# Optimization experiments

Hardware: AMD Instinct MI355X
Metric: run time of the kernel (lower is better)

The kernel has to match this reference:

```python
import jax, jax.numpy as jnp
import numpy as np

N_NODES = 50000
N_EDGES = 400000
IN_F, HID_F, OUT_F = 768, 16, 21


def setup_inputs() -> dict:
    key = jax.random.key(0)
    ks = jax.random.split(key, 7)
    feature = jax.random.normal(ks[0], (N_NODES, IN_F), dtype=jnp.float32)
    W1 = jax.random.normal(ks[1], (IN_F, HID_F), dtype=jnp.float32) * 0.03
    b1 = jax.random.normal(ks[2], (HID_F,), dtype=jnp.float32) * 0.01
    W2 = jax.random.normal(ks[3], (HID_F, OUT_F), dtype=jnp.float32) * 0.1
    b2 = jax.random.normal(ks[4], (OUT_F,), dtype=jnp.float32) * 0.01
    src = jax.random.randint(ks[5], (N_EDGES,), 0, N_NODES, dtype=jnp.int32)
    dst = jax.random.randint(ks[6], (N_EDGES,), 0, N_NODES, dtype=jnp.int32)
    return {"feature": feature, "W1": W1, "b1": b1, "W2": W2, "b2": b2,
            "src": src, "dst": dst}


def _gcn_agg(h, src, dst):
    # copy_src + sum reduce: gather source features along edges, scatter-add to dst
    return jax.ops.segment_sum(h[src], dst, num_segments=N_NODES)


def reference(feature, W1, b1, W2, b2, src, dst):
    # layer 1: aggregate then linear + relu
    h = _gcn_agg(feature, src, dst)            # [N, 768]
    h = jax.nn.relu(h @ W1 + b1)               # [N, 16]
    # layer 2: aggregate then linear (no activation)
    h = _gcn_agg(h, src, dst)                  # [N, 16]
    return h @ W2 + b2                         # [N, 21]
```

## Files before the change

### kernel.cpp

```cpp
#include <hip/hip_runtime.h>

#define NN 50000
#define NE 400000
#define INF 768
#define HF 16
#define OF 21
#define ELLW 40

#define FMA4(ACC, SS, VV) { (ACC).x += (SS)*(VV).x; (ACC).y += (SS)*(VV).y; \
                            (ACC).z += (SS)*(VV).z; (ACC).w += (SS)*(VV).w; }

__global__ __launch_bounds__(256) void scatter_kernel(const int* __restrict__ src,
                                                      const int* __restrict__ dst,
                                                      int* __restrict__ cnt,
                                                      int* __restrict__ ell) {
    int e = blockIdx.x * 256 + threadIdx.x;
    if (e >= NE) return;
    int d = dst[e];
    int pos = atomicAdd(&cnt[d], 1);
    if (pos < ELLW) ell[d * ELLW + pos] = src[e];
}

__global__ __launch_bounds__(256, 3) void gemm1_kernel(const float* __restrict__ F,
                                                       const float* __restrict__ W1,
                                                       float* __restrict__ P) {
    const int tid = threadIdx.x;
    const int wv = tid >> 6, lane = tid & 63;
    const int g = lane >> 4;
    const int u = lane & 15;
    const int ks = u >> 2;
    const int jq = u & 3;
    const int koff = g * 16 + ks * 4;
    const int rowbase = blockIdx.x * 32 + wv * 8;

    int roff[8];
#pragma unroll
    for (int r = 0; r < 8; ++r) {
        int row = rowbase + r;
        if (row > NN - 1) row = NN - 1;
        roff[r] = row * INF + koff;
    }

    const float* wbase = W1 + koff * HF + jq * 4;

    float4 acc[8];
#pragma unroll
    for (int r = 0; r < 8; ++r) acc[r] = make_float4(0.f, 0.f, 0.f, 0.f);

#pragma unroll 1
    for (int t = 0; t < INF / 64; ++t) {
        const float* wp = wbase + t * 64 * HF;
        const float4 w0 = *(const float4*)(wp + 0 * HF);
        const float4 w1 = *(const float4*)(wp + 1 * HF);
        const float4 w2 = *(const float4*)(wp + 2 * HF);
        const float4 w3 = *(const float4*)(wp + 3 * HF);
#pragma unroll
        for (int r = 0; r < 8; ++r) {
            const float4 f = *(const float4*)(F + roff[r] + t * 64);
            FMA4(acc[r], f.x, w0);
            FMA4(acc[r], f.y, w1);
            FMA4(acc[r], f.z, w2);
            FMA4(acc[r], f.w, w3);
        }
    }

#pragma unroll
    for (int r = 0; r < 8; ++r) {
        float4 v = acc[r];
#define RED(X) { v.X += __shfl_xor(v.X, 4);  v.X += __shfl_xor(v.X, 8); \
                 v.X += __shfl_xor(v.X, 16); v.X += __shfl_xor(v.X, 32); }
        RED(x) RED(y) RED(z) RED(w)
#undef RED
        const int row = rowbase + r;
        if (lane < 4 && row < NN)
            *(float4*)(P + (size_t)row * HF + jq * 4) = v;
    }
}

__global__ __launch_bounds__(256) void agg1_kernel(const float* __restrict__ P,
                                                   const int* __restrict__ cnt,
                                                   const int* __restrict__ ell,
                                                   float* __restrict__ A1) {
    int g = blockIdx.x * 256 + threadIdx.x;
    int node = g >> 4;
    if (node >= NN) return;
    const int l = g & 15, es = l >> 2, q = l & 3;
    int c = cnt[node]; if (c > ELLW) c = ELLW;
    const int* ep = ell + node * ELLW;

    float4 v = {0,0,0,0};
    for (int i = es; i < c; i += 4) {
        int s = ep[i];
        float4 p = *(const float4*)(P + (size_t)s * HF + q * 4);
        v.x += p.x; v.y += p.y; v.z += p.z; v.w += p.w;
    }
#define BFLY2(VAL) { VAL += __shfl_xor(VAL, 4); VAL += __shfl_xor(VAL, 8); }
    BFLY2(v.x) BFLY2(v.y) BFLY2(v.z) BFLY2(v.w)
#undef BFLY2
    if (es == 0)
        *(float4*)(A1 + (size_t)node * HF + q * 4) = v;
}

__global__ __launch_bounds__(256) void agg2out_kernel(const float* __restrict__ A1,
                                                      const float* __restrict__ b1,
                                                      const int* __restrict__ cnt,
                                                      const int* __restrict__ ell,
                                                      const float* __restrict__ W2,
                                                      const float* __restrict__ b2,
                                                      float* __restrict__ out) {
    __shared__ float W2s[HF * OF];
    __shared__ float b2s[OF];
    const int t = threadIdx.x;
    for (int i = t; i < HF * OF; i += 256) W2s[i] = W2[i];
    if (t < OF) b2s[t] = b2[t];
    __syncthreads();

    int g = blockIdx.x * 256 + t;
    int node = g >> 4;
    if (node >= NN) return;
    const int l = g & 15, es = l >> 2, q = l & 3;

    const float4 bb = *(const float4*)(b1 + q * 4);
    int c = cnt[node]; if (c > ELLW) c = ELLW;
    const int* ep = ell + node * ELLW;

    float4 v = {0,0,0,0};
    for (int i = es; i < c; i += 4) {
        int s = ep[i];
        float4 h = *(const float4*)(A1 + (size_t)s * HF + q * 4);
        h.x = fmaxf(h.x + bb.x, 0.0f);
        h.y = fmaxf(h.y + bb.y, 0.0f);
        h.z = fmaxf(h.z + bb.z, 0.0f);
        h.w = fmaxf(h.w + bb.w, 0.0f);
        v.x += h.x; v.y += h.y; v.z += h.z; v.w += h.w;
    }
#define BFLY2(VAL) { VAL += __shfl_xor(VAL, 4); VAL += __shfl_xor(VAL, 8); }
    BFLY2(v.x) BFLY2(v.y) BFLY2(v.z) BFLY2(v.w)
#undef BFLY2

    const float* w0 = W2s + (q * 4 + 0) * OF;
    const float* w1 = W2s + (q * 4 + 1) * OF;
    const float* w2 = W2s + (q * 4 + 2) * OF;
    const float* w3 = W2s + (q * 4 + 3) * OF;
    float o[OF];
#pragma unroll
    for (int cc = 0; cc < OF; ++cc)
        o[cc] = v.x * w0[cc] + v.y * w1[cc] + v.z * w2[cc] + v.w * w3[cc];
#pragma unroll
    for (int cc = 0; cc < OF; ++cc) {
        o[cc] += __shfl_xor(o[cc], 1);
        o[cc] += __shfl_xor(o[cc], 2);
    }
    if (es == 0) {
        float* op = out + (size_t)node * OF;
        for (int cc = q; cc < OF; cc += 4) op[cc] = o[cc] + b2s[cc];
    }
}

extern "C" void kernel_launch(void* const* d_in, const int* in_sizes, int n_in,
                              void* d_out, int out_size, void* d_ws, size_t ws_size,
                              hipStream_t stream) {
    const float* F   = (const float*)d_in[0];
    const float* W1  = (const float*)d_in[1];
    const float* b1  = (const float*)d_in[2];
    const float* W2  = (const float*)d_in[3];
    const float* b2  = (const float*)d_in[4];
    const int*   src = (const int*)d_in[5];
    const int*   dst = (const int*)d_in[6];
    float* out = (float*)d_out;

    char* ws = (char*)d_ws;
    int*   cnt = (int*)(ws);
    int*   ell = (int*)(ws + 200192);
    float* P   = (float*)(ws + 8200192);
    float* A1  = (float*)(ws + 11400192);

    (void)hipMemsetAsync(cnt, 0, NN * sizeof(int), stream);
    scatter_kernel<<<(NE + 255) / 256, 256, 0, stream>>>(src, dst, cnt, ell);
    gemm1_kernel<<<(NN + 31) / 32, 256, 0, stream>>>(F, W1, P);
    agg1_kernel<<<(NN * 16 + 255) / 256, 256, 0, stream>>>(P, cnt, ell, A1);
    agg2out_kernel<<<(NN * 16 + 255) / 256, 256, 0, stream>>>(A1, b1, cnt, ell, W2, b2, out);
}
```

Before: 300.4 us.

## Stage W1 in LDS and software-pipeline feature loads in gemm1

gemm1 now loads all of W1 into shared memory once per block, using a permuted layout so each lane reads its weights with contiguous float4 accesses. Blocks grow to 512 threads, with each wave handling 4 rows instead of 8. The k loop is restructured so that 16 float4 feature loads are issued a whole stage ahead of the FMAs that consume them, aiming to hide HBM latency on the bandwidth-bound 153MB feature read. The costs are 48KB of LDS per block, which limits occupancy, and a larger register footprint.

```diff
diff --git a/kernel.cpp b/kernel.cpp
--- a/kernel.cpp
+++ b/kernel.cpp
@@ -21,51 +21,88 @@
     if (pos < ELLW) ell[d * ELLW + pos] = src[e];
 }
 
-__global__ __launch_bounds__(256, 3) void gemm1_kernel(const float* __restrict__ F,
+__global__ __launch_bounds__(512, 4) void gemm1_kernel(const float* __restrict__ F,
                                                        const float* __restrict__ W1,
                                                        float* __restrict__ P) {
+    __shared__ float Ws[INF * HF];
+
     const int tid = threadIdx.x;
+    for (int i = tid; i < (INF * HF) / 4; i += 512) {
+        const int k = i >> 2, jq = i & 3;
+        const int dg = (k & 3) * 768 + (k >> 6) * 64 + (((k >> 4) & 3) << 4)
+                     + (((k >> 2) & 3) << 2) + jq;
+        *(float4*)(Ws + dg * 4) = *(const float4*)(W1 + i * 4);
+    }
+    __syncthreads();
+
     const int wv = tid >> 6, lane = tid & 63;
-    const int g = lane >> 4;
-    const int u = lane & 15;
-    const int ks = u >> 2;
-    const int jq = u & 3;
-    const int koff = g * 16 + ks * 4;
-    const int rowbase = blockIdx.x * 32 + wv * 8;
-
-    int roff[8];
-#pragma unroll
-    for (int r = 0; r < 8; ++r) {
+    const int jq = lane & 3;
+    const int koff = lane & 60;
+    const int rowbase = blockIdx.x * 32 + wv * 4;
+
+    int roff[4];
+#pragma unroll
+    for (int r = 0; r < 4; ++r) {
         int row = rowbase + r;
         if (row > NN - 1) row = NN - 1;
         roff[r] = row * INF + koff;
     }
 
-    const float* wbase = W1 + koff * HF + jq * 4;
-
-    float4 acc[8];
-#pragma unroll
-    for (int r = 0; r < 8; ++r) acc[r] = make_float4(0.f, 0.f, 0.f, 0.f);
+    const float* lw = Ws + lane * 4;
+
+    float4 acc[4];
+#pragma unroll
+    for (int r = 0; r < 4; ++r) acc[r] = make_float4(0.f, 0.f, 0.f, 0.f);
+
+    float4 q[4][4];
+#pragma unroll
+    for (int j = 0; j < 4; ++j)
+#pragma unroll
+        for (int r = 0; r < 4; ++r)
+            q[j][r] = *(const float4*)(F + roff[r] + j * 64);
 
 #pragma unroll 1
-    for (int t = 0; t < INF / 64; ++t) {
-        const float* wp = wbase + t * 64 * HF;
-        const float4 w0 = *(const float4*)(wp + 0 * HF);
-        const float4 w1 = *(const float4*)(wp + 1 * HF);
-        const float4 w2 = *(const float4*)(wp + 2 * HF);
-        const float4 w3 = *(const float4*)(wp + 3 * HF);
-#pragma unroll
-        for (int r = 0; r < 8; ++r) {
-            const float4 f = *(const float4*)(F + roff[r] + t * 64);
-            FMA4(acc[r], f.x, w0);
-            FMA4(acc[r], f.y, w1);
-            FMA4(acc[r], f.z, w2);
-            FMA4(acc[r], f.w, w3);
+    for (int g4 = 0; g4 < 2; ++g4) {
+        const float* lwg = lw + g4 * 1024;
+        const int foff = g4 * 256 + 256;
+#pragma unroll
+        for (int j = 0; j < 4; ++j) {
+            const float4 w0 = *(const float4*)(lwg + j * 256 + 0 * 3072);
+            const float4 w1 = *(const float4*)(lwg + j * 256 + 1 * 3072);
+            const float4 w2 = *(const float4*)(lwg + j * 256 + 2 * 3072);
+            const float4 w3 = *(const float4*)(lwg + j * 256 + 3 * 3072);
+#pragma unroll
+            for (int r = 0; r < 4; ++r) {
+                FMA4(acc[r], q[j][r].x, w0);
+                FMA4(acc[r], q[j][r].y, w1);
+                FMA4(acc[r], q[j][r].z, w2);
+                FMA4(acc[r], q[j][r].w, w3);
+            }
+#pragma unroll
+            for (int r = 0; r < 4; ++r)
+                q[j][r] = *(const float4*)(F + roff[r] + foff + j * 64);
         }
     }
-
-#pragma unroll
-    for (int r = 0; r < 8; ++r) {
+    {
+        const float* lwg = lw + 2048;
+#pragma unroll
+        for (int j = 0; j < 4; ++j) {
+            const float4 w0 = *(const float4*)(lwg + j * 256 + 0 * 3072);
+            const float4 w1 = *(const float4*)(lwg + j * 256 + 1 * 3072);
+            const float4 w2 = *(const float4*)(lwg + j * 256 + 2 * 3072);
+            const float4 w3 = *(const float4*)(lwg + j * 256 + 3 * 3072);
+#pragma unroll
+            for (int r = 0; r < 4; ++r) {
+                FMA4(acc[r], q[j][r].x, w0);
+                FMA4(acc[r], q[j][r].y, w1);
+                FMA4(acc[r], q[j][r].z, w2);
+                FMA4(acc[r], q[j][r].w, w3);
+            }
+        }
+    }
+
+#pragma unroll
+    for (int r = 0; r < 4; ++r) {
         float4 v = acc[r];
 #define RED(X) { v.X += __shfl_xor(v.X, 4);  v.X += __shfl_xor(v.X, 8); \
                  v.X += __shfl_xor(v.X, 16); v.X += __shfl_xor(v.X, 32); }
@@ -177,7 +214,7 @@
 
     (void)hipMemsetAsync(cnt, 0, NN * sizeof(int), stream);
     scatter_kernel<<<(NE + 255) / 256, 256, 0, stream>>>(src, dst, cnt, ell);
-    gemm1_kernel<<<(NN + 31) / 32, 256, 0, stream>>>(F, W1, P);
+    gemm1_kernel<<<(NN + 31) / 32, 512, 0, stream>>>(F, W1, P);
     agg1_kernel<<<(NN * 16 + 255) / 256, 256, 0, stream>>>(P, cnt, ell, A1);
     agg2out_kernel<<<(NN * 16 + 255) / 256, 256, 0, stream>>>(A1, b1, cnt, ell, W2, b2, out);
 }
```

New measurement: 353.7 us. 17.7% more time.

## Stage feature tiles into LDS via async global_load_lds with double buffering

Applied to the files above, without the earlier changes.

The projection GEMM now puts the whole W1 matrix into shared memory in a permuted layout, then streams 64x64 feature tiles into double-buffered LDS with direct global-to-LDS loads, prefetching the next tile while computing the current one. Blocks grow to 512 threads covering 64 rows. The goal is to hide the latency of the large feature read (about 150 MB, memory-bound) and stop reloading W1 from global memory. The cost is about 80 KB of LDS per block, which limits occupancy, plus a block-wide barrier every iteration.

```diff
diff --git a/kernel.cpp b/kernel.cpp
--- a/kernel.cpp
+++ b/kernel.cpp
@@ -21,47 +21,75 @@
     if (pos < ELLW) ell[d * ELLW + pos] = src[e];
 }
 
-__global__ __launch_bounds__(256, 3) void gemm1_kernel(const float* __restrict__ F,
+__device__ __forceinline__ void gload_lds16(const float* g, float* l) {
+    __builtin_amdgcn_global_load_lds(
+        (const __attribute__((address_space(1))) unsigned int*)g,
+        (__attribute__((address_space(3))) unsigned int*)l,
+        16, 0, 0);
+}
+
+__global__ __launch_bounds__(512, 2) void gemm1_kernel(const float* __restrict__ F,
                                                        const float* __restrict__ W1,
                                                        float* __restrict__ P) {
+    __shared__ float Ws[INF * HF];
+    __shared__ float Fb[2][64 * 64];
+
     const int tid = threadIdx.x;
+    for (int i = tid; i < (INF * HF) / 4; i += 512) {
+        const int k = i >> 2, jq = i & 3;
+        const int dg = (k & 3) * 768 + (k >> 6) * 64 + (((k >> 4) & 3) << 4)
+                     + (((k >> 2) & 3) << 2) + jq;
+        *(float4*)(Ws + dg * 4) = *(const float4*)(W1 + i * 4);
+    }
+
     const int wv = tid >> 6, lane = tid & 63;
-    const int g = lane >> 4;
-    const int u = lane & 15;
-    const int ks = u >> 2;
-    const int jq = u & 3;
-    const int koff = g * 16 + ks * 4;
-    const int rowbase = blockIdx.x * 32 + wv * 8;
-
-    int roff[8];
-#pragma unroll
-    for (int r = 0; r < 8; ++r) {
-        int row = rowbase + r;
-        if (row > NN - 1) row = NN - 1;
-        roff[r] = row * INF + koff;
-    }
-
-    const float* wbase = W1 + koff * HF + jq * 4;
+    const int jq = lane & 3;
+    const int koff = lane & 60;
+    const int rowbase = blockIdx.x * 64;
+
+    const int colb = (lane & 15) * 4;
+    int srow0 = rowbase + wv * 8 + 0 + (lane >> 4);
+    int srow1 = rowbase + wv * 8 + 4 + (lane >> 4);
+    if (srow0 > NN - 1) srow0 = NN - 1;
+    if (srow1 > NN - 1) srow1 = NN - 1;
+    const float* sp0 = F + (size_t)srow0 * INF + colb;
+    const float* sp1 = F + (size_t)srow1 * INF + colb;
+    float* ld0a = &Fb[0][wv * 512];        float* ld0b = &Fb[0][wv * 512 + 256];
+    float* ld1a = &Fb[1][wv * 512];        float* ld1b = &Fb[1][wv * 512 + 256];
+
+    gload_lds16(sp0, ld0a);
+    gload_lds16(sp1, ld0b);
+
+    const float* lw = Ws + lane * 4;
 
     float4 acc[8];
 #pragma unroll
     for (int r = 0; r < 8; ++r) acc[r] = make_float4(0.f, 0.f, 0.f, 0.f);
 
+    __syncthreads();
+
 #pragma unroll 1
-    for (int t = 0; t < INF / 64; ++t) {
-        const float* wp = wbase + t * 64 * HF;
-        const float4 w0 = *(const float4*)(wp + 0 * HF);
-        const float4 w1 = *(const float4*)(wp + 1 * HF);
-        const float4 w2 = *(const float4*)(wp + 2 * HF);
-        const float4 w3 = *(const float4*)(wp + 3 * HF);
+    for (int t = 0; t < 12; ++t) {
+        if (t < 11) {
+            const int c = (t + 1) * 64;
+            if ((t & 1) == 0) { gload_lds16(sp0 + c, ld1a); gload_lds16(sp1 + c, ld1b); }
+            else              { gload_lds16(sp0 + c, ld0a); gload_lds16(sp1 + c, ld0b); }
+        }
+        const float* lwt = lw + t * 256;
+        const float4 w0 = *(const float4*)(lwt + 0 * 3072);
+        const float4 w1 = *(const float4*)(lwt + 1 * 3072);
+        const float4 w2 = *(const float4*)(lwt + 2 * 3072);
+        const float4 w3 = *(const float4*)(lwt + 3 * 3072);
+        const float* fb = &Fb[t & 1][koff];
 #pragma unroll
         for (int r = 0; r < 8; ++r) {
-            const float4 f = *(const float4*)(F + roff[r] + t * 64);
+            const float4 f = *(const float4*)(fb + (wv * 8 + r) * 64);
             FMA4(acc[r], f.x, w0);
             FMA4(acc[r], f.y, w1);
             FMA4(acc[r], f.z, w2);
             FMA4(acc[r], f.w, w3);
         }
+        __syncthreads();
     }
 
 #pragma unroll
@@ -71,7 +99,7 @@
                  v.X += __shfl_xor(v.X, 16); v.X += __shfl_xor(v.X, 32); }
         RED(x) RED(y) RED(z) RED(w)
 #undef RED
-        const int row = rowbase + r;
+        const int row = rowbase + wv * 8 + r;
         if (lane < 4 && row < NN)
             *(float4*)(P + (size_t)row * HF + jq * 4) = v;
     }
@@ -177,7 +205,7 @@
 
     (void)hipMemsetAsync(cnt, 0, NN * sizeof(int), stream);
     scatter_kernel<<<(NE + 255) / 256, 256, 0, stream>>>(src, dst, cnt, ell);
-    gemm1_kernel<<<(NN + 31) / 32, 256, 0, stream>>>(F, W1, P);
+    gemm1_kernel<<<(NN + 63) / 64, 512, 0, stream>>>(F, W1, P);
     agg1_kernel<<<(NN * 16 + 255) / 256, 256, 0, stream>>>(P, cnt, ell, A1);
     agg2out_kernel<<<(NN * 16 + 255) / 256, 256, 0, stream>>>(A1, b1, cnt, ell, W2, b2, out);
 }
```

Result: no change. 300.6 us (+0.1%).
